# Performance work log

Hardware: AMD Instinct MI355X
Metric: run time of the kernel (lower is better)

## Reference

```python
import jax, jax.numpy as jnp
import numpy as np

N_SRC = 100000
N_DST = 100000
E = 1250000
IN_SRC = 64
IN_DST = 64
OUT = 64


def setup_inputs() -> dict:
    key = jax.random.key(0)
    k = jax.random.split(key, 7)
    x_src = jax.random.normal(k[0], (N_SRC, IN_SRC), dtype=jnp.float32)
    x_dst = jax.random.normal(k[1], (N_DST, IN_DST), dtype=jnp.float32)
    edge_index_sd = jax.random.randint(k[2], (2, E), 0, N_SRC, dtype=jnp.int64)
    edge_weight = jax.random.uniform(k[3], (E,), dtype=jnp.float32)
    # Linear params (torch: y = x @ W.T + b), kaiming-ish scale
    W_nei = jax.random.normal(k[4], (OUT, IN_SRC), dtype=jnp.float32) / np.sqrt(IN_SRC)
    W_self = jax.random.normal(k[5], (OUT, IN_DST), dtype=jnp.float32) / np.sqrt(IN_DST)
    b_self = jax.random.normal(k[6], (OUT,), dtype=jnp.float32) / np.sqrt(IN_DST)
    return {"x_src": x_src, "x_dst": x_dst, "edge_index_sd": edge_index_sd,
            "edge_weight": edge_weight, "W_nei": W_nei, "W_self": W_self,
            "b_self": b_self}


def reference(x_src, x_dst, edge_index_sd, edge_weight, W_nei, W_self, b_self):
    src_idx = edge_index_sd[0]
    dst_idx = edge_index_sd[1]
    # self term: [N_dst, out]
    out = x_dst @ W_self.T + b_self
    # neighbor transform then gather per edge: [E, out]
    h_src = x_src @ W_nei.T
    msg = h_src[src_idx] * edge_weight[:, None]
    # scatter-add into dst rows
    out = out.at[dst_idx].add(msg)
    return out
```

## Files before the change

kernel.cpp:

```cpp
#include <hip/hip_runtime.h>

#define NN 100000
#define FD 64
#define NE 1250000

#define RPB 128
#define NBK ((NN + RPB - 1) / RPB)
#define NBP 1024
#define CAP 2048
#define CH  8192
#define NCH ((NE + CH - 1) / CH)
#define NTILE (NN / 16)

#define TPW 2
#define NWM (NTILE / TPW)
#define LIN_GRID ((2 * NWM + 3) / 4)

typedef __attribute__((ext_vector_type(8))) short bf16x8;
typedef __attribute__((ext_vector_type(4))) float f32x4;

__device__ __forceinline__ short cvt_bf16(float f) {
    unsigned u = __float_as_uint(f);
    return (short)((u + 0x7FFFu + ((u >> 16) & 1u)) >> 16);
}
__device__ __forceinline__ float bf2f(unsigned short u) {
    return __uint_as_float(((unsigned)u) << 16);
}

__global__ __launch_bounds__(256) void lin_both(
    const float* __restrict__ x_src, const float* __restrict__ x_dst,
    const float* __restrict__ W_nei, const float* __restrict__ W_self,
    const float* __restrict__ b_self, unsigned short* __restrict__ hbuf,
    float* __restrict__ out)
{
    const int lane = threadIdx.x & 63;
    const int m    = lane & 15;
    const int quad = lane >> 4;
    const int gw   = blockIdx.x * 4 + (threadIdx.x >> 6);
    if (gw >= 2 * NWM) return;
    const bool self = gw >= NWM;
    const int  wm   = self ? gw - NWM : gw;
    const float* __restrict__ x = self ? x_dst : x_src;
    const float* __restrict__ W = self ? W_self : W_nei;

    const float* xb = x + (size_t)(wm * (TPW * 16) + m) * FD;
    float4 xv[TPW][4];
    #pragma unroll
    for (int t = 0; t < TPW; t++) {
        const float* xr = xb + (size_t)t * 16 * FD;
        xv[t][0] = *(const float4*)(xr + quad * 8);
        xv[t][1] = *(const float4*)(xr + quad * 8 + 4);
        xv[t][2] = *(const float4*)(xr + 32 + quad * 8);
        xv[t][3] = *(const float4*)(xr + 32 + quad * 8 + 4);
    }

    bf16x8 wf[2][4];
    #pragma unroll
    for (int kc = 0; kc < 2; kc++) {
        #pragma unroll
        for (int ct = 0; ct < 4; ct++) {
            const float4 w0 = *(const float4*)(W + (ct * 16 + m) * FD + kc * 32 + quad * 8);
            const float4 w1 = *(const float4*)(W + (ct * 16 + m) * FD + kc * 32 + quad * 8 + 4);
            bf16x8 f;
            f[0]=cvt_bf16(w0.x); f[1]=cvt_bf16(w0.y); f[2]=cvt_bf16(w0.z); f[3]=cvt_bf16(w0.w);
            f[4]=cvt_bf16(w1.x); f[5]=cvt_bf16(w1.y); f[6]=cvt_bf16(w1.z); f[7]=cvt_bf16(w1.w);
            wf[kc][ct] = f;
        }
    }

    float4 bv[4];
    if (self) {
        #pragma unroll
        for (int ct = 0; ct < 4; ct++)
            bv[ct] = *(const float4*)(b_self + ct * 16 + quad * 4);
    }

    #pragma unroll
    for (int t = 0; t < TPW; t++) {
        bf16x8 a0, a1;
        a0[0]=cvt_bf16(xv[t][0].x); a0[1]=cvt_bf16(xv[t][0].y);
        a0[2]=cvt_bf16(xv[t][0].z); a0[3]=cvt_bf16(xv[t][0].w);
        a0[4]=cvt_bf16(xv[t][1].x); a0[5]=cvt_bf16(xv[t][1].y);
        a0[6]=cvt_bf16(xv[t][1].z); a0[7]=cvt_bf16(xv[t][1].w);
        a1[0]=cvt_bf16(xv[t][2].x); a1[1]=cvt_bf16(xv[t][2].y);
        a1[2]=cvt_bf16(xv[t][2].z); a1[3]=cvt_bf16(xv[t][2].w);
        a1[4]=cvt_bf16(xv[t][3].x); a1[5]=cvt_bf16(xv[t][3].y);
        a1[6]=cvt_bf16(xv[t][3].z); a1[7]=cvt_bf16(xv[t][3].w);

        f32x4 acc[4];
        #pragma unroll
        for (int ct = 0; ct < 4; ct++) {
            f32x4 z = (f32x4){0.f, 0.f, 0.f, 0.f};
            z = __builtin_amdgcn_mfma_f32_16x16x32_bf16(wf[0][ct], a0, z, 0, 0, 0);
            z = __builtin_amdgcn_mfma_f32_16x16x32_bf16(wf[1][ct], a1, z, 0, 0, 0);
            acc[ct] = z;
        }

        const size_t rowbase = (size_t)(wm * (TPW * 16) + t * 16 + m) * FD;
        if (!self) {
            #pragma unroll
            for (int ct = 0; ct < 4; ct++) {
                ushort4 sv;
                sv.x = (unsigned short)cvt_bf16(acc[ct][0]);
                sv.y = (unsigned short)cvt_bf16(acc[ct][1]);
                sv.z = (unsigned short)cvt_bf16(acc[ct][2]);
                sv.w = (unsigned short)cvt_bf16(acc[ct][3]);
                *(ushort4*)(hbuf + rowbase + ct * 16 + quad * 4) = sv;
            }
        } else {
            #pragma unroll
            for (int ct = 0; ct < 4; ct++) {
                float4 v;
                v.x = acc[ct][0] + bv[ct].x;
                v.y = acc[ct][1] + bv[ct].y;
                v.z = acc[ct][2] + bv[ct].z;
                v.w = acc[ct][3] + bv[ct].w;
                *(float4*)(out + rowbase + ct * 16 + quad * 4) = v;
            }
        }
    }
}

__global__ __launch_bounds__(1024) void kplace(
    const int* __restrict__ src, const int* __restrict__ dst,
    const float* __restrict__ ew, int* __restrict__ gcursor,
    int2* __restrict__ sp)
{
    __shared__ int cnt[NBP];
    const int t = threadIdx.x;
    if (t < NBP) cnt[t] = 0;
    __syncthreads();
    const int e0 = blockIdx.x * CH;

    int d[8];
    #pragma unroll
    for (int k = 0; k < 8; k++) {
        const int e = e0 + t + k * 1024;
        d[k] = (e < NE) ? dst[e] : -1;
    }
    #pragma unroll
    for (int k = 0; k < 8; k++)
        if (d[k] >= 0) atomicAdd(&cnt[d[k] >> 7], 1);
    __syncthreads();

    if (t < NBP) {
        const int c = cnt[t];
        cnt[t] = c ? (t * CAP + atomicAdd(&gcursor[t], c)) : 0;
    }
    __syncthreads();

    int s[8]; float w[8];
    #pragma unroll
    for (int k = 0; k < 8; k++) {
        const int e = e0 + t + k * 1024;
        if (e < NE) { s[k] = src[e]; w[k] = ew[e]; }
    }
    #pragma unroll
    for (int k = 0; k < 8; k++) {
        if (d[k] >= 0) {
            const int p = atomicAdd(&cnt[d[k] >> 7], 1);
            sp[p] = make_int2(s[k] | ((d[k] & (RPB - 1)) << 17),
                              __float_as_int(w[k]));
        }
    }
}

__global__ __launch_bounds__(256) void ksub(
    const int2* __restrict__ sp, const int* __restrict__ gcursor,
    int2* __restrict__ sp2, int* __restrict__ rowstart,
    int* __restrict__ rowend)
{
    __shared__ int hist[RPB];
    __shared__ int cur[RPB];
    const int t = threadIdx.x;
    const int b = blockIdx.x;
    const int s0 = b * CAP;
    const int s1 = s0 + gcursor[b];
    if (t < RPB) hist[t] = 0;
    __syncthreads();
    for (int j = s0 + t; j < s1; j += 256)
        atomicAdd(&hist[sp[j].x >> 17], 1);
    __syncthreads();
    if (t < 64) {
        const int v0 = hist[2*t], v1 = hist[2*t + 1];
        const int s = v0 + v1;
        int inc = s;
        #pragma unroll
        for (int off = 1; off < 64; off <<= 1) {
            int u = __shfl_up(inc, off, 64);
            if (t >= off) inc += u;
        }
        const int ex = inc - s;
        cur[2*t]     = s0 + ex;
        cur[2*t + 1] = s0 + ex + v0;
    }
    __syncthreads();
    const int row0 = b * RPB;
    if (t < RPB && row0 + t < NN) {
        rowstart[row0 + t] = cur[t];
        rowend[row0 + t]   = cur[t] + hist[t];
    }
    __syncthreads();
    for (int j = s0 + t; j < s1; j += 256) {
        const int2 q = sp[j];
        const int p = atomicAdd(&cur[q.x >> 17], 1);
        sp2[p] = q;
    }
}

__global__ __launch_bounds__(256) void gather_rows(
    const unsigned short* __restrict__ h, const int* __restrict__ rowstart,
    const int* __restrict__ rowend, const int2* __restrict__ sp2,
    float* __restrict__ out)
{
    const int lane = threadIdx.x & 63;
    const int q    = lane >> 4;
    const int t    = lane & 15;
    const int row  = (int)((blockIdx.x * blockDim.x + threadIdx.x) >> 6);
    if (row >= NN) return;
    const int j0 = rowstart[row];
    const int n  = rowend[row] - j0;
    const unsigned tb = (unsigned)t << 3;
    float a0 = 0.f, a1 = 0.f, a2 = 0.f, a3 = 0.f;

    for (int kb = 0; kb < n; kb += 64) {
        const int rem = n - kb;
        const int m   = rem < 64 ? rem : 64;
        int2 qv = make_int2(0, 0);
        if (lane < m) qv = sp2[j0 + kb + lane];
        for (int k = 0; k < m; k += 16) {
            uint2 dv[4]; float wv[4];
            #pragma unroll
            for (int j = 0; j < 4; j++) {
                const int kk = k + j * 4 + q;
                const int ax = __shfl(qv.x, kk, 64);
                const int ay = __shfl(qv.y, kk, 64);
                const unsigned off = (((unsigned)(ax & 0x1FFFF)) << 7) | tb;
                wv[j] = __int_as_float(ay);
                dv[j] = *(const uint2*)((const char*)h + off);
            }
            #pragma unroll
            for (int j = 0; j < 4; j++) {
                const float w = wv[j];
                a0 = fmaf(__uint_as_float(dv[j].x << 16),         w, a0);
                a1 = fmaf(__uint_as_float(dv[j].x & 0xFFFF0000u), w, a1);
                a2 = fmaf(__uint_as_float(dv[j].y << 16),         w, a2);
                a3 = fmaf(__uint_as_float(dv[j].y & 0xFFFF0000u), w, a3);
            }
        }
    }
    a0 += __shfl_xor(a0, 16, 64); a1 += __shfl_xor(a1, 16, 64);
    a2 += __shfl_xor(a2, 16, 64); a3 += __shfl_xor(a3, 16, 64);
    a0 += __shfl_xor(a0, 32, 64); a1 += __shfl_xor(a1, 32, 64);
    a2 += __shfl_xor(a2, 32, 64); a3 += __shfl_xor(a3, 32, 64);
    if (q == 0) {
        float4* p = (float4*)(out + (size_t)row * FD + (t << 2));
        float4 v = *p;
        v.x += a0; v.y += a1; v.z += a2; v.w += a3;
        *p = v;
    }
}

__global__ __launch_bounds__(256) void scatter_edges(
    const unsigned short* __restrict__ h, const int* __restrict__ eidx,
    const float* __restrict__ ew, float* __restrict__ out)
{
    const int lane  = threadIdx.x & 63;
    const int gwave = (int)((blockIdx.x * blockDim.x + threadIdx.x) >> 6);
    const int nwave = (int)((gridDim.x * blockDim.x) >> 6);
    const int* __restrict__ src = eidx;
    const int* __restrict__ dst = eidx + NE;
    for (int e = gwave; e < NE; e += nwave) {
        const float v = bf2f(h[(size_t)src[e] * FD + lane]) * ew[e];
        atomicAdd(out + (size_t)dst[e] * FD + lane, v);
    }
}

extern "C" void kernel_launch(void* const* d_in, const int* in_sizes, int n_in,
                              void* d_out, int out_size, void* d_ws, size_t ws_size,
                              hipStream_t stream)
{
    const float* x_src  = (const float*)d_in[0];
    const float* x_dst  = (const float*)d_in[1];
    const int*   eidx   = (const int*)  d_in[2];
    const float* ew     = (const float*)d_in[3];
    const float* W_nei  = (const float*)d_in[4];
    const float* W_self = (const float*)d_in[5];
    const float* b_self = (const float*)d_in[6];
    float* out = (float*)d_out;

    const int* src = eidx;
    const int* dst = eidx + NE;

    char* ws = (char*)d_ws;
    size_t off = 0;
    auto alloc = [&](size_t bytes) { char* p = ws + off; off += (bytes + 15) & ~(size_t)15; return p; };
    unsigned short* h = (unsigned short*)alloc((size_t)NN * FD * sizeof(unsigned short));
    int*  gcursor  = (int*) alloc((size_t)NBP * sizeof(int));
    int*  rowstart = (int*) alloc((size_t)NN * sizeof(int));
    int*  rowend   = (int*) alloc((size_t)NN * sizeof(int));
    int2* sp       = (int2*)alloc((size_t)NBP * CAP * sizeof(int2));
    int2* sp2      = (int2*)alloc((size_t)NBP * CAP * sizeof(int2));
    const size_t need_main = off;
    const size_t need_h    = (size_t)NN * FD * sizeof(unsigned short);

    if (ws_size >= need_main) {
        hipMemsetAsync(gcursor, 0, (size_t)NBP * sizeof(int), stream);
        lin_both<<<LIN_GRID, 256, 0, stream>>>(x_src, x_dst, W_nei, W_self,
                                               b_self, h, out);
        kplace<<<NCH, 1024, 0, stream>>>(src, dst, ew, gcursor, sp);
        ksub  <<<NBK, 256, 0, stream>>>(sp, gcursor, sp2, rowstart, rowend);
        gather_rows<<<(NN * 64 + 255) / 256, 256, 0, stream>>>(h, rowstart,
                                                               rowend, sp2, out);
    } else if (ws_size >= need_h) {
        lin_both<<<LIN_GRID, 256, 0, stream>>>(x_src, x_dst, W_nei, W_self,
                                               b_self, h, out);
        scatter_edges<<<2048, 256, 0, stream>>>(h, eidx, ew, out);
    }
}
```

Baseline: 186.4 us.

## Fuse bucket sort and row gather into one LDS-resident kernel

Merges the per-bucket counting sort (ksub) and the row-wise gather into one kernel, sort_gather. Each 512-thread block sorts its bucket's edges into shared memory and then gathers the 128 destination rows directly from LDS. This removes the sp2/rowstart/rowend global round trip and one launch. The gcursor memset moves into block 0 of lin_both, which removes the separate memset call. In exchange, each block now handles 128 rows with only 8 waves, so skewed buckets can serialize work and occupancy drops because of the roughly 16KB LDS buffer per block.

```diff
diff --git a/kernel.cpp b/kernel.cpp
--- a/kernel.cpp
+++ b/kernel.cpp
@@ -31,8 +31,12 @@
     const float* __restrict__ x_src, const float* __restrict__ x_dst,
     const float* __restrict__ W_nei, const float* __restrict__ W_self,
     const float* __restrict__ b_self, unsigned short* __restrict__ hbuf,
-    float* __restrict__ out)
-{
+    float* __restrict__ out, int* __restrict__ gcur)
+{
+    if (gcur && blockIdx.x == 0) {
+        #pragma unroll
+        for (int i = 0; i < NBP / 256; i++) gcur[threadIdx.x + i * 256] = 0;
+    }
     const int lane = threadIdx.x & 63;
     const int m    = lane & 15;
     const int quad = lane >> 4;
@@ -165,21 +169,32 @@
     }
 }
 
-__global__ __launch_bounds__(256) void ksub(
+__global__ __launch_bounds__(512) void sort_gather(
     const int2* __restrict__ sp, const int* __restrict__ gcursor,
-    int2* __restrict__ sp2, int* __restrict__ rowstart,
-    int* __restrict__ rowend)
-{
+    const unsigned short* __restrict__ h, float* __restrict__ out)
+{
+    __shared__ int2 ebuf[CAP + 16];
     __shared__ int hist[RPB];
+    __shared__ int rs[RPB];
     __shared__ int cur[RPB];
     const int t = threadIdx.x;
     const int b = blockIdx.x;
+    const int cnt = gcursor[b];
     const int s0 = b * CAP;
-    const int s1 = s0 + gcursor[b];
+
     if (t < RPB) hist[t] = 0;
-    __syncthreads();
-    for (int j = s0 + t; j < s1; j += 256)
-        atomicAdd(&hist[sp[j].x >> 17], 1);
+
+    int2 ev[4]; int er[4];
+    #pragma unroll
+    for (int k = 0; k < 4; k++) {
+        const int j = t + k * 512;
+        if (j < cnt) { ev[k] = sp[s0 + j]; er[k] = ev[k].x >> 17; }
+        else er[k] = -1;
+    }
+    __syncthreads();
+    #pragma unroll
+    for (int k = 0; k < 4; k++)
+        if (er[k] >= 0) atomicAdd(&hist[er[k]], 1);
     __syncthreads();
     if (t < 64) {
         const int v0 = hist[2*t], v1 = hist[2*t + 1];
@@ -191,73 +206,65 @@
             if (t >= off) inc += u;
         }
         const int ex = inc - s;
-        cur[2*t]     = s0 + ex;
-        cur[2*t + 1] = s0 + ex + v0;
-    }
-    __syncthreads();
+        rs[2*t]      = ex;       cur[2*t]     = ex;
+        rs[2*t + 1]  = ex + v0;  cur[2*t + 1] = ex + v0;
+    }
+    __syncthreads();
+    #pragma unroll
+    for (int k = 0; k < 4; k++) {
+        if (er[k] >= 0) {
+            const int p = atomicAdd(&cur[er[k]], 1);
+            ebuf[p] = ev[k];
+        }
+    }
+    if (t < 16) ebuf[cnt + t] = make_int2(0, 0);
+    __syncthreads();
+
+    const int wv   = t >> 6;
+    const int lane = t & 63;
+    const int q    = lane >> 4;
+    const int tc   = lane & 15;
+    const unsigned tb = (unsigned)tc << 3;
     const int row0 = b * RPB;
-    if (t < RPB && row0 + t < NN) {
-        rowstart[row0 + t] = cur[t];
-        rowend[row0 + t]   = cur[t] + hist[t];
-    }
-    __syncthreads();
-    for (int j = s0 + t; j < s1; j += 256) {
-        const int2 q = sp[j];
-        const int p = atomicAdd(&cur[q.x >> 17], 1);
-        sp2[p] = q;
-    }
-}
-
-__global__ __launch_bounds__(256) void gather_rows(
-    const unsigned short* __restrict__ h, const int* __restrict__ rowstart,
-    const int* __restrict__ rowend, const int2* __restrict__ sp2,
-    float* __restrict__ out)
-{
-    const int lane = threadIdx.x & 63;
-    const int q    = lane >> 4;
-    const int t    = lane & 15;
-    const int row  = (int)((blockIdx.x * blockDim.x + threadIdx.x) >> 6);
-    if (row >= NN) return;
-    const int j0 = rowstart[row];
-    const int n  = rowend[row] - j0;
-    const unsigned tb = (unsigned)t << 3;
-    float a0 = 0.f, a1 = 0.f, a2 = 0.f, a3 = 0.f;
-
-    for (int kb = 0; kb < n; kb += 64) {
-        const int rem = n - kb;
-        const int m   = rem < 64 ? rem : 64;
-        int2 qv = make_int2(0, 0);
-        if (lane < m) qv = sp2[j0 + kb + lane];
-        for (int k = 0; k < m; k += 16) {
-            uint2 dv[4]; float wv[4];
+
+    for (int i = 0; i < 16; i++) {
+        const int r   = wv + i * 8;
+        const int row = row0 + r;
+        if (row >= NN) break;
+        const int rsr = rs[r];
+        const int n   = hist[r];
+        float a0 = 0.f, a1 = 0.f, a2 = 0.f, a3 = 0.f;
+        for (int k = 0; k < n; k += 16) {
+            int2 ed[4];
+            #pragma unroll
+            for (int j = 0; j < 4; j++)
+                ed[j] = ebuf[rsr + k + j * 4 + q];
+            uint2 dv[4]; float wv4[4];
             #pragma unroll
             for (int j = 0; j < 4; j++) {
-                const int kk = k + j * 4 + q;
-                const int ax = __shfl(qv.x, kk, 64);
-                const int ay = __shfl(qv.y, kk, 64);
-                const unsigned off = (((unsigned)(ax & 0x1FFFF)) << 7) | tb;
-                wv[j] = __int_as_float(ay);
+                const unsigned off = (((unsigned)(ed[j].x & 0x1FFFF)) << 7) | tb;
                 dv[j] = *(const uint2*)((const char*)h + off);
+                wv4[j] = (k + j * 4 + q < n) ? __int_as_float(ed[j].y) : 0.f;
             }
             #pragma unroll
             for (int j = 0; j < 4; j++) {
-                const float w = wv[j];
+                const float w = wv4[j];
                 a0 = fmaf(__uint_as_float(dv[j].x << 16),         w, a0);
                 a1 = fmaf(__uint_as_float(dv[j].x & 0xFFFF0000u), w, a1);
                 a2 = fmaf(__uint_as_float(dv[j].y << 16),         w, a2);
                 a3 = fmaf(__uint_as_float(dv[j].y & 0xFFFF0000u), w, a3);
             }
         }
-    }
-    a0 += __shfl_xor(a0, 16, 64); a1 += __shfl_xor(a1, 16, 64);
-    a2 += __shfl_xor(a2, 16, 64); a3 += __shfl_xor(a3, 16, 64);
-    a0 += __shfl_xor(a0, 32, 64); a1 += __shfl_xor(a1, 32, 64);
-    a2 += __shfl_xor(a2, 32, 64); a3 += __shfl_xor(a3, 32, 64);
-    if (q == 0) {
-        float4* p = (float4*)(out + (size_t)row * FD + (t << 2));
-        float4 v = *p;
-        v.x += a0; v.y += a1; v.z += a2; v.w += a3;
-        *p = v;
+        a0 += __shfl_xor(a0, 16, 64); a1 += __shfl_xor(a1, 16, 64);
+        a2 += __shfl_xor(a2, 16, 64); a3 += __shfl_xor(a3, 16, 64);
+        a0 += __shfl_xor(a0, 32, 64); a1 += __shfl_xor(a1, 32, 64);
+        a2 += __shfl_xor(a2, 32, 64); a3 += __shfl_xor(a3, 32, 64);
+        if (q == 0) {
+            float4* p = (float4*)(out + (size_t)row * FD + (tc << 2));
+            float4 v = *p;
+            v.x += a0; v.y += a1; v.z += a2; v.w += a3;
+            *p = v;
+        }
     }
 }
 
@@ -297,24 +304,18 @@
     auto alloc = [&](size_t bytes) { char* p = ws + off; off += (bytes + 15) & ~(size_t)15; return p; };
     unsigned short* h = (unsigned short*)alloc((size_t)NN * FD * sizeof(unsigned short));
     int*  gcursor  = (int*) alloc((size_t)NBP * sizeof(int));
-    int*  rowstart = (int*) alloc((size_t)NN * sizeof(int));
-    int*  rowend   = (int*) alloc((size_t)NN * sizeof(int));
     int2* sp       = (int2*)alloc((size_t)NBP * CAP * sizeof(int2));
-    int2* sp2      = (int2*)alloc((size_t)NBP * CAP * sizeof(int2));
     const size_t need_main = off;
     const size_t need_h    = (size_t)NN * FD * sizeof(unsigned short);
 
     if (ws_size >= need_main) {
-        hipMemsetAsync(gcursor, 0, (size_t)NBP * sizeof(int), stream);
         lin_both<<<LIN_GRID, 256, 0, stream>>>(x_src, x_dst, W_nei, W_self,
-                                               b_self, h, out);
+                                               b_self, h, out, gcursor);
         kplace<<<NCH, 1024, 0, stream>>>(src, dst, ew, gcursor, sp);
-        ksub  <<<NBK, 256, 0, stream>>>(sp, gcursor, sp2, rowstart, rowend);
-        gather_rows<<<(NN * 64 + 255) / 256, 256, 0, stream>>>(h, rowstart,
-                                                               rowend, sp2, out);
+        sort_gather<<<NBK, 512, 0, stream>>>(sp, gcursor, h, out);
     } else if (ws_size >= need_h) {
         lin_both<<<LIN_GRID, 256, 0, stream>>>(x_src, x_dst, W_nei, W_self,
-                                               b_self, h, out);
+                                               b_self, h, out, nullptr);
         scatter_edges<<<2048, 256, 0, stream>>>(h, eidx, ew, out);
     }
 }
```

After: 172.1 us. 7.7% less time.
